# Performance work log

Measured on AMD Instinct MI355X. Metric: run time of the kernel, lower is better.

## Reference

```python
import jax, jax.numpy as jnp
import numpy as np

NUM_EXPERTS = 8
CAPACITY = 320  # per-batch per-expert token capacity


def setup_inputs() -> dict:
    key = jax.random.key(0)
    k0, k1, k2, k3 = jax.random.split(key, 4)
    B, S, D, F = 4, 2048, 1024, 4096
    E = NUM_EXPERTS
    hidden_states = jax.random.normal(k0, (B, S, D), dtype=jnp.float32)
    gate_w = jax.random.normal(k1, (E, D), dtype=jnp.float32) * 0.02
    w1 = jax.random.normal(k2, (E, D, F), dtype=jnp.float32) * 0.02
    w2 = jax.random.normal(k3, (E, F, D), dtype=jnp.float32) * 0.02
    return {"hidden_states": hidden_states, "gate_w": gate_w, "w1": w1, "w2": w2}


def reference(hidden_states, gate_w, w1, w2):
    E, C = NUM_EXPERTS, CAPACITY
    B, S, D = hidden_states.shape

    # --- route ---
    router_logits = jnp.einsum('bsd,ed->bse', hidden_states, gate_w)
    router_probs = jax.nn.softmax(router_logits, axis=-1)
    expert_idx = jnp.argmax(router_probs, axis=-1)                      # [B,S]
    onehot = jax.nn.one_hot(expert_idx, E, dtype=jnp.int32)             # [B,S,E]
    priority = jnp.cumsum(onehot, axis=1)                               # [B,S,E]
    router_mask = onehot * (priority <= C)                              # [B,S,E]
    assigned = jnp.sum(router_mask, axis=-1) > 0                        # [B,S]
    # slot within expert buffer; dropped tokens go to overflow slot C
    slot = jnp.where(assigned, jnp.sum(priority * onehot, axis=-1) - 1, C)  # [B,S]
    top_prob = jnp.max(router_probs, axis=-1, keepdims=True)            # [B,S,1]

    # --- dispatch: scatter tokens into [B,E,C+1,D] buffers ---
    def dispatch(x_b, e_b, s_b):
        return jnp.zeros((E, C + 1, D), x_b.dtype).at[e_b, s_b].set(x_b)
    buf = jax.vmap(dispatch)(hidden_states, expert_idx, slot)           # [B,E,C+1,D]

    # --- per-expert FFN as grouped GEMM ---
    h = jax.nn.silu(jnp.einsum('becd,edf->becf', buf, w1))
    y = jnp.einsum('becf,efd->becd', h, w2)                             # [B,E,C+1,D]

    # --- combine: gather expert outputs back to token order ---
    gathered = jax.vmap(lambda y_b, e_b, s_b: y_b[e_b, s_b])(y, expert_idx, slot)  # [B,S,D]
    next_states = jnp.where(assigned[..., None], gathered, hidden_states)
    out = top_prob * next_states

    # argmax of capacity-masked one-hot: dropped tokens -> expert 0
    expert_index = jnp.where(assigned, expert_idx, 0)
    return out, router_logits, expert_index
```

## Files before the change

kernel.cpp:

```cpp
#include <hip/hip_runtime.h>

#define B_  4
#define S_  2048
#define D_  1024
#define F_  4096
#define E_  8
#define C_  320
#define MPAD_ 1280
#define NT_ (B_*S_)
#define SLOT_ 49152

typedef short bf16x8 __attribute__((ext_vector_type(8)));
typedef float f32x4  __attribute__((ext_vector_type(4)));

using gptr_t = const __attribute__((address_space(1))) void*;
using lptr_t = __attribute__((address_space(3))) void*;

__device__ static inline void gll16(const void* g, void* l) {
    __builtin_amdgcn_global_load_lds((gptr_t)g, (lptr_t)l, 16, 0, 0);
}

__device__ static inline unsigned short f2b(float f) {
    unsigned int u = __float_as_uint(f);
    u += 0x7fffu + ((u >> 16) & 1u);
    return (unsigned short)(u >> 16);
}

__global__ __launch_bounds__(256) void k_convT(const float* __restrict__ in,
                                               unsigned short* __restrict__ out,
                                               int R, int Cc) {
    __shared__ unsigned short ld[64][66];
    int e = blockIdx.z;
    const float* src = in + (size_t)e * R * Cc;
    unsigned short* dst = out + (size_t)e * R * Cc;
    int c0 = blockIdx.x * 64, r0 = blockIdx.y * 64;
    int t = threadIdx.x;

    int rr = t >> 4;
    int cg = t & 15;
#pragma unroll
    for (int p = 0; p < 4; p++) {
        int row = p * 16 + rr;
        float4 v = *(const float4*)(src + (size_t)(r0 + row) * Cc + c0 + cg * 4);
        ld[cg * 4 + 0][row] = f2b(v.x);
        ld[cg * 4 + 1][row] = f2b(v.y);
        ld[cg * 4 + 2][row] = f2b(v.z);
        ld[cg * 4 + 3][row] = f2b(v.w);
    }
    __syncthreads();

    int cc = t >> 3;
    int rg = t & 7;
#pragma unroll
    for (int p = 0; p < 2; p++) {
        int col = p * 32 + cc;
        const unsigned* lp = (const unsigned*)&ld[col][rg * 8];
        uint4 w;
        w.x = lp[0]; w.y = lp[1]; w.z = lp[2]; w.w = lp[3];
        *(uint4*)(dst + (size_t)(c0 + col) * R + r0 + rg * 8) = w;
    }
}

__global__ __launch_bounds__(256) void k_router(const float* __restrict__ hs,
                                                const float* __restrict__ gw,
                                                float* __restrict__ logits,
                                                int* __restrict__ eidx,
                                                float* __restrict__ tp) {
    int tok  = (int)((blockIdx.x * 256 + threadIdx.x) >> 6);
    int lane = threadIdx.x & 63;
    const float* x = hs + (size_t)tok * D_;
    double acc[E_];
#pragma unroll
    for (int e = 0; e < E_; e++) acc[e] = 0.0;
    for (int i = 0; i < 16; i++) {
        float xv = x[lane + 64 * i];
#pragma unroll
        for (int e = 0; e < E_; e++)
            acc[e] += (double)xv * (double)gw[e * D_ + lane + 64 * i];
    }
#pragma unroll
    for (int e = 0; e < E_; e++) {
#pragma unroll
        for (int off = 32; off > 0; off >>= 1)
            acc[e] += __shfl_xor(acc[e], off, 64);
    }
    if (lane == 0) {
        float l[E_];
        float mx = -1e30f; int am = 0;
#pragma unroll
        for (int e = 0; e < E_; e++) {
            l[e] = (float)acc[e];
            if (l[e] > mx) { mx = l[e]; am = e; }
        }
        float se = 0.f;
#pragma unroll
        for (int e = 0; e < E_; e++) se += __expf(l[e] - mx);
        tp[tok]   = 1.0f / se;
        eidx[tok] = am;
#pragma unroll
        for (int e = 0; e < E_; e++) logits[(size_t)tok * E_ + e] = l[e];
    }
}

__global__ __launch_bounds__(256) void k_scan(const int* __restrict__ eidx,
                                              int* __restrict__ slot,
                                              int* __restrict__ tok_list,
                                              int* __restrict__ counts,
                                              float* __restrict__ eif) {
    int b = blockIdx.x;
    __shared__ int cCnt[32][E_];
    __shared__ int cBase[32][E_];
    int t = threadIdx.x, wv = t >> 6, lane = t & 63;
    const int* eb = eidx + b * S_;
    for (int c = wv; c < 32; c += 4) {
        int e = eb[c * 64 + lane];
#pragma unroll
        for (int x = 0; x < E_; x++) {
            unsigned long long m = __ballot(e == x);
            if (lane == 0) cCnt[c][x] = __popcll(m);
        }
    }
    __syncthreads();
    if (t < E_) {
        int s = 0;
        for (int c = 0; c < 32; c++) { cBase[c][t] = s; s += cCnt[c][t]; }
        counts[b * E_ + t] = s;
    }
    __syncthreads();
    for (int c = wv; c < 32; c += 4) {
        int s_tok = c * 64 + lane;
        int e = eb[s_tok];
        unsigned long long lowmask = (1ull << lane) - 1ull;
        int rank = 0;
#pragma unroll
        for (int x = 0; x < E_; x++) {
            unsigned long long m = __ballot(e == x);
            if (x == e) rank = __popcll(m & lowmask);
        }
        int pos = cBase[c][e] + rank;
        int assigned = (pos < C_);
        slot[b * S_ + s_tok] = assigned ? pos : C_;
        if (assigned) tok_list[(b * E_ + e) * C_ + pos] = s_tok;
        eif[b * S_ + s_tok] = assigned ? (float)e : 0.0f;
    }
}

__global__ void k_base(const int* __restrict__ counts,
                       int* __restrict__ ebase,
                       int* __restrict__ nE) {
    int e = threadIdx.x;
    if (e < E_) {
        int s = 0;
#pragma unroll
        for (int b = 0; b < B_; b++) {
            ebase[b * E_ + e] = s;
            s += min(counts[b * E_ + e], C_);
        }
        nE[e] = s;
    }
}

__global__ __launch_bounds__(256) void k_dispatch(const float* __restrict__ hs,
                                                  const int* __restrict__ tlB,
                                                  const int* __restrict__ ebase,
                                                  const int* __restrict__ nE,
                                                  int* __restrict__ tlG,
                                                  unsigned short* __restrict__ Xd) {
    int w    = (int)((blockIdx.x * 256 + threadIdx.x) >> 6);
    int lane = threadIdx.x & 63;
    int e = w / MPAD_, r = w - e * MPAD_;
    unsigned short* drow = Xd + ((size_t)e * MPAD_ + r) * D_;
    if (r < nE[e]) {
        int b = 0;
#pragma unroll
        for (int bb = 1; bb < B_; bb++) if (r >= ebase[bb * E_ + e]) b = bb;
        int pos = r - ebase[b * E_ + e];
        int ts  = tlB[(b * E_ + e) * C_ + pos];
        if (lane == 0) tlG[e * MPAD_ + r] = b * S_ + ts;
        const float* src = hs + ((size_t)b * S_ + ts) * D_;
#pragma unroll
        for (int i = 0; i < 2; i++) {
            int c0 = (lane + 64 * i) * 8;
            float4 v0 = *(const float4*)(src + c0);
            float4 v1 = *(const float4*)(src + c0 + 4);
            uint4 pk;
            pk.x = (unsigned)f2b(v0.x) | ((unsigned)f2b(v0.y) << 16);
            pk.y = (unsigned)f2b(v0.z) | ((unsigned)f2b(v0.w) << 16);
            pk.z = (unsigned)f2b(v1.x) | ((unsigned)f2b(v1.y) << 16);
            pk.w = (unsigned)f2b(v1.z) | ((unsigned)f2b(v1.w) << 16);
            *(uint4*)(drow + c0) = pk;
        }
    } else {
        uint4 zz = {0u, 0u, 0u, 0u};
#pragma unroll
        for (int i = 0; i < 2; i++)
            *(uint4*)(drow + (lane + 64 * i) * 8) = zz;
    }
}

template<int LDK, int KT>
__device__ __forceinline__ void gemm_core(const unsigned short* __restrict__ Ab,
                                          const unsigned short* __restrict__ Bb,
                                          char* sm, f32x4 (&acc)[4][4]) {
    const int t    = threadIdx.x;
    const int lane = t & 63;
    const int wv   = t >> 6;
    const int wm   = wv >> 1;
    const int wn   = wv & 1;

    const int sr  = t >> 3;
    const int scs = (t & 7) ^ (sr & 7);
    const unsigned short* aS = Ab + (size_t)sr * LDK + scs * 8;
    const unsigned short* bS = Bb + (size_t)sr * LDK + scs * 8;
    const int wvoff = wv * 1024;

    const int rl  = lane & 15;
    const int sw  = lane & 7;
    const int kg  = lane >> 4;
    const int sx0 = ((kg    ) ^ sw) << 4;
    const int sx1 = ((kg + 4) ^ sw) << 4;
    const int aro = (wm * 64 + rl) * 128;
    const int bro = (wn * 64 + rl) * 128;

#pragma unroll
    for (int g = 0; g < 2; g++) {
        char* L = sm + g * SLOT_;
        const unsigned short* aP = aS + (size_t)g * 64;
        const unsigned short* bP = bS + (size_t)g * 64;
#pragma unroll
        for (int j = 0; j < 4; j++) gll16(aP + (size_t)j * 64 * LDK, L + j * 8192 + wvoff);
#pragma unroll
        for (int j = 0; j < 2; j++) gll16(bP + (size_t)j * 64 * LDK, L + 32768 + j * 8192 + wvoff);
    }
    asm volatile("s_waitcnt vmcnt(6)" ::: "memory");
    __builtin_amdgcn_s_barrier();

    int cslot = 0;
#pragma unroll 1
    for (int kt = 0; kt < KT; ++kt) {
        const char* cs = sm + cslot * SLOT_;
        int ps = cslot + 2; if (ps >= 3) ps -= 3;
        char* L = sm + ps * SLOT_;

        if (kt + 2 < KT) {
            const unsigned short* aP = aS + (size_t)(kt + 2) * 64;
            const unsigned short* bP = bS + (size_t)(kt + 2) * 64;
#pragma unroll
            for (int j = 0; j < 4; j++) gll16(aP + (size_t)j * 64 * LDK, L + j * 8192 + wvoff);
#pragma unroll
            for (int j = 0; j < 2; j++) gll16(bP + (size_t)j * 64 * LDK, L + 32768 + j * 8192 + wvoff);
        }

        bf16x8 a0[4], b0[4], a1[4], b1[4];
#pragma unroll
        for (int i = 0; i < 4; i++) a0[i] = *(const bf16x8*)(cs + aro + i * 2048 + sx0);
#pragma unroll
        for (int j = 0; j < 4; j++) b0[j] = *(const bf16x8*)(cs + 32768 + bro + j * 2048 + sx0);
#pragma unroll
        for (int i = 0; i < 4; i++) a1[i] = *(const bf16x8*)(cs + aro + i * 2048 + sx1);
#pragma unroll
        for (int j = 0; j < 4; j++) b1[j] = *(const bf16x8*)(cs + 32768 + bro + j * 2048 + sx1);

        __builtin_amdgcn_s_setprio(1);
#pragma unroll
        for (int i = 0; i < 4; i++)
#pragma unroll
            for (int j = 0; j < 4; j++)
                acc[i][j] = __builtin_amdgcn_mfma_f32_16x16x32_bf16(a0[i], b0[j], acc[i][j], 0, 0, 0);
#pragma unroll
        for (int i = 0; i < 4; i++)
#pragma unroll
            for (int j = 0; j < 4; j++)
                acc[i][j] = __builtin_amdgcn_mfma_f32_16x16x32_bf16(a1[i], b1[j], acc[i][j], 0, 0, 0);
        __builtin_amdgcn_s_setprio(0);

        if (kt + 2 < KT)      { asm volatile("s_waitcnt vmcnt(6)" ::: "memory"); }
        else if (kt + 1 < KT) { asm volatile("s_waitcnt vmcnt(0)" ::: "memory"); }
        __builtin_amdgcn_s_barrier();

        cslot++; if (cslot >= 3) cslot = 0;
    }
}

__global__ __launch_bounds__(512, 2) void k_ffn1(const unsigned short* __restrict__ Xd,
                                                 const unsigned short* __restrict__ w1t,
                                                 const int* __restrict__ nE,
                                                 unsigned short* __restrict__ h) {
    __shared__ __align__(16) char sm[3 * SLOT_];
    int id  = blockIdx.x;
    int e   = id & 7;
    int rem = id >> 3;
    int mt  = rem % 5;
    int nt  = rem / 5;
    int m0  = mt * 256;
    if (m0 >= nE[e]) return;
    int n0  = nt * 128;

    f32x4 acc[4][4];
    f32x4 z = {0.f, 0.f, 0.f, 0.f};
#pragma unroll
    for (int i = 0; i < 4; i++)
#pragma unroll
        for (int j = 0; j < 4; j++) acc[i][j] = z;

    const unsigned short* Ab = Xd  + ((size_t)e * MPAD_ + m0) * D_;
    const unsigned short* Bb = w1t + ((size_t)e * F_    + n0) * D_;
    gemm_core<D_, D_ / 64>(Ab, Bb, sm, acc);

    int lane = threadIdx.x & 63, wv = threadIdx.x >> 6, wm = wv >> 1, wn = wv & 1;
    unsigned short* hb = h + (size_t)e * MPAD_ * F_;
    int rb = m0 + wm * 64 + ((lane >> 4) << 2);
    int cb = n0 + wn * 64 + (lane & 15);
#pragma unroll
    for (int i = 0; i < 4; i++)
#pragma unroll
        for (int r = 0; r < 4; r++) {
            unsigned short* hr = hb + (size_t)(rb + i * 16 + r) * F_ + cb;
#pragma unroll
            for (int j = 0; j < 4; j++) {
                float v = acc[i][j][r];
                v = v / (1.0f + __expf(-v));
                hr[j * 16] = f2b(v);
            }
        }
}

__global__ __launch_bounds__(512, 2) void k_ffn2(const unsigned short* __restrict__ h,
                                                 const unsigned short* __restrict__ w2t,
                                                 const int* __restrict__ nE,
                                                 const int* __restrict__ tlG,
                                                 const float* __restrict__ tp,
                                                 float* __restrict__ out) {
    __shared__ __align__(16) char sm[3 * SLOT_];
    int id  = blockIdx.x;
    int e   = id & 7;
    int rem = id >> 3;
    int mt  = rem % 5;
    int nt  = rem / 5;
    int m0  = mt * 256;
    int n   = nE[e];
    if (m0 >= n) return;
    int n0  = nt * 128;

    f32x4 acc[4][4];
    f32x4 z = {0.f, 0.f, 0.f, 0.f};
#pragma unroll
    for (int i = 0; i < 4; i++)
#pragma unroll
        for (int j = 0; j < 4; j++) acc[i][j] = z;

    const unsigned short* Ab = h   + ((size_t)e * MPAD_ + m0) * F_;
    const unsigned short* Bb = w2t + ((size_t)e * D_    + n0) * F_;
    gemm_core<F_, F_ / 64>(Ab, Bb, sm, acc);

    int lane = threadIdx.x & 63, wv = threadIdx.x >> 6, wm = wv >> 1, wn = wv & 1;
    const int* tl = tlG + e * MPAD_;
    int rb = m0 + wm * 64 + ((lane >> 4) << 2);
    int cb = n0 + wn * 64 + (lane & 15);
#pragma unroll
    for (int i = 0; i < 4; i++)
#pragma unroll
        for (int r = 0; r < 4; r++) {
            int row = rb + i * 16 + r;
            if (row < n) {
                int gt = tl[row];
                float sc = tp[gt];
                float* orow = out + (size_t)gt * D_ + cb;
#pragma unroll
                for (int j = 0; j < 4; j++)
                    orow[j * 16] = sc * acc[i][j][r];
            }
        }
}

__global__ __launch_bounds__(256) void k_pass(const float* __restrict__ hs,
                                              const int* __restrict__ slot,
                                              const float* __restrict__ tp,
                                              float* __restrict__ out) {
    int tok  = (int)((blockIdx.x * 256 + threadIdx.x) >> 6);
    int lane = threadIdx.x & 63;
    if (slot[tok] < C_) return;
    float sc = tp[tok];
    const float* src = hs + (size_t)tok * D_;
    float* dst = out + (size_t)tok * D_;
#pragma unroll
    for (int i = 0; i < 4; i++) {
        float4 v = *(const float4*)(src + (lane + 64 * i) * 4);
        v.x *= sc; v.y *= sc; v.z *= sc; v.w *= sc;
        *(float4*)(dst + (lane + 64 * i) * 4) = v;
    }
}

extern "C" void kernel_launch(void* const* d_in, const int* in_sizes, int n_in,
                              void* d_out, int out_size, void* d_ws, size_t ws_size,
                              hipStream_t stream) {
    const float* hs = (const float*)d_in[0];
    const float* gw = (const float*)d_in[1];
    const float* w1 = (const float*)d_in[2];
    const float* w2 = (const float*)d_in[3];

    float* out    = (float*)d_out;
    float* logits = out + (size_t)NT_ * D_;
    float* eif    = logits + (size_t)NT_ * E_;

    char* ws = (char*)d_ws;
    int*            eidx   = (int*)(ws + 0);
    int*            slot   = (int*)(ws + 65536);
    float*          tp     = (float*)(ws + 131072);
    int*            tlB    = (int*)(ws + 196608);
    int*            tlG    = (int*)(ws + 237568);
    int*            counts = (int*)(ws + 278528);
    int*            ebase  = (int*)(ws + 278784);
    int*            nE     = (int*)(ws + 279040);
    unsigned short* Xd     = (unsigned short*)(ws + 327680);
    unsigned short* w1t    = (unsigned short*)(ws + 33554432ull);
    unsigned short* w2t    = (unsigned short*)(ws + 100663296ull);
    unsigned short* hbuf   = (unsigned short*)(ws + 167772160ull);

    dim3 blk(256);
    k_convT<<<dim3(F_ / 64, D_ / 64, E_), blk, 0, stream>>>(w1, w1t, D_, F_);
    k_convT<<<dim3(D_ / 64, F_ / 64, E_), blk, 0, stream>>>(w2, w2t, F_, D_);
    k_router<<<dim3(NT_ / 4), blk, 0, stream>>>(hs, gw, logits, eidx, tp);
    k_scan<<<dim3(B_), blk, 0, stream>>>(eidx, slot, tlB, counts, eif);
    k_base<<<dim3(1), dim3(64), 0, stream>>>(counts, ebase, nE);
    k_dispatch<<<dim3(E_ * MPAD_ / 4), blk, 0, stream>>>(hs, tlB, ebase, nE, tlG, Xd);
    k_ffn1<<<dim3(1280), dim3(512), 0, stream>>>(Xd, w1t, nE, hbuf);
    k_ffn2<<<dim3(320), dim3(512), 0, stream>>>(hbuf, w2t, nE, tlG, tp, out);
    k_pass<<<dim3(NT_ / 4), blk, 0, stream>>>(hs, slot, tp, out);
}
```

Measured before the change: 588.3 us.

## Replace triple-buffered 256x128 GEMM tiles with single-buffer 128x128 tiles

Measured after the change: 536.2 us. -8.9%, faster.

```diff
diff --git a/kernel.cpp b/kernel.cpp
--- a/kernel.cpp
+++ b/kernel.cpp
@@ -8,7 +8,6 @@
 #define C_  320
 #define MPAD_ 1280
 #define NT_ (B_*S_)
-#define SLOT_ 49152
 
 typedef short bf16x8 __attribute__((ext_vector_type(8)));
 typedef float f32x4  __attribute__((ext_vector_type(4)));
@@ -212,6 +211,8 @@
     const int scs = (t & 7) ^ (sr & 7);
     const unsigned short* aS = Ab + (size_t)sr * LDK + scs * 8;
     const unsigned short* bS = Bb + (size_t)sr * LDK + scs * 8;
+    char* ldsA = sm;
+    char* ldsB = sm + 16384;
     const int wvoff = wv * 1024;
 
     const int rl  = lane & 15;
@@ -222,77 +223,50 @@
     const int aro = (wm * 64 + rl) * 128;
     const int bro = (wn * 64 + rl) * 128;
 
-#pragma unroll
-    for (int g = 0; g < 2; g++) {
-        char* L = sm + g * SLOT_;
-        const unsigned short* aP = aS + (size_t)g * 64;
-        const unsigned short* bP = bS + (size_t)g * 64;
-#pragma unroll
-        for (int j = 0; j < 4; j++) gll16(aP + (size_t)j * 64 * LDK, L + j * 8192 + wvoff);
-#pragma unroll
-        for (int j = 0; j < 2; j++) gll16(bP + (size_t)j * 64 * LDK, L + 32768 + j * 8192 + wvoff);
-    }
-    asm volatile("s_waitcnt vmcnt(6)" ::: "memory");
-    __builtin_amdgcn_s_barrier();
-
-    int cslot = 0;
 #pragma unroll 1
     for (int kt = 0; kt < KT; ++kt) {
-        const char* cs = sm + cslot * SLOT_;
-        int ps = cslot + 2; if (ps >= 3) ps -= 3;
-        char* L = sm + ps * SLOT_;
-
-        if (kt + 2 < KT) {
-            const unsigned short* aP = aS + (size_t)(kt + 2) * 64;
-            const unsigned short* bP = bS + (size_t)(kt + 2) * 64;
-#pragma unroll
-            for (int j = 0; j < 4; j++) gll16(aP + (size_t)j * 64 * LDK, L + j * 8192 + wvoff);
-#pragma unroll
-            for (int j = 0; j < 2; j++) gll16(bP + (size_t)j * 64 * LDK, L + 32768 + j * 8192 + wvoff);
-        }
-
-        bf16x8 a0[4], b0[4], a1[4], b1[4];
-#pragma unroll
-        for (int i = 0; i < 4; i++) a0[i] = *(const bf16x8*)(cs + aro + i * 2048 + sx0);
-#pragma unroll
-        for (int j = 0; j < 4; j++) b0[j] = *(const bf16x8*)(cs + 32768 + bro + j * 2048 + sx0);
-#pragma unroll
-        for (int i = 0; i < 4; i++) a1[i] = *(const bf16x8*)(cs + aro + i * 2048 + sx1);
-#pragma unroll
-        for (int j = 0; j < 4; j++) b1[j] = *(const bf16x8*)(cs + 32768 + bro + j * 2048 + sx1);
-
-        __builtin_amdgcn_s_setprio(1);
+        __syncthreads();
+        const unsigned short* aP = aS + kt * 64;
+        const unsigned short* bP = bS + kt * 64;
+#pragma unroll
+        for (int j = 0; j < 4; j++) gll16(aP + (size_t)(j * 32) * LDK, ldsA + j * 4096 + wvoff);
+#pragma unroll
+        for (int j = 0; j < 4; j++) gll16(bP + (size_t)(j * 32) * LDK, ldsB + j * 4096 + wvoff);
+        __syncthreads();
+
+        bf16x8 a[4], b[4];
+#pragma unroll
+        for (int i = 0; i < 4; i++) a[i] = *(const bf16x8*)(ldsA + aro + i * 2048 + sx0);
+#pragma unroll
+        for (int j = 0; j < 4; j++) b[j] = *(const bf16x8*)(ldsB + bro + j * 2048 + sx0);
 #pragma unroll
         for (int i = 0; i < 4; i++)
 #pragma unroll
             for (int j = 0; j < 4; j++)
-                acc[i][j] = __builtin_amdgcn_mfma_f32_16x16x32_bf16(a0[i], b0[j], acc[i][j], 0, 0, 0);
+                acc[i][j] = __builtin_amdgcn_mfma_f32_16x16x32_bf16(a[i], b[j], acc[i][j], 0, 0, 0);
+#pragma unroll
+        for (int i = 0; i < 4; i++) a[i] = *(const bf16x8*)(ldsA + aro + i * 2048 + sx1);
+#pragma unroll
+        for (int j = 0; j < 4; j++) b[j] = *(const bf16x8*)(ldsB + bro + j * 2048 + sx1);
 #pragma unroll
         for (int i = 0; i < 4; i++)
 #pragma unroll
             for (int j = 0; j < 4; j++)
-                acc[i][j] = __builtin_amdgcn_mfma_f32_16x16x32_bf16(a1[i], b1[j], acc[i][j], 0, 0, 0);
-        __builtin_amdgcn_s_setprio(0);
-
-        if (kt + 2 < KT)      { asm volatile("s_waitcnt vmcnt(6)" ::: "memory"); }
-        else if (kt + 1 < KT) { asm volatile("s_waitcnt vmcnt(0)" ::: "memory"); }
-        __builtin_amdgcn_s_barrier();
-
-        cslot++; if (cslot >= 3) cslot = 0;
-    }
-}
-
-__global__ __launch_bounds__(512, 2) void k_ffn1(const unsigned short* __restrict__ Xd,
+                acc[i][j] = __builtin_amdgcn_mfma_f32_16x16x32_bf16(a[i], b[j], acc[i][j], 0, 0, 0);
+    }
+}
+
+__global__ __launch_bounds__(256, 4) void k_ffn1(const unsigned short* __restrict__ Xd,
                                                  const unsigned short* __restrict__ w1t,
                                                  const int* __restrict__ nE,
                                                  unsigned short* __restrict__ h) {
-    __shared__ __align__(16) char sm[3 * SLOT_];
+    __shared__ __align__(16) char sm[32768];
     int id  = blockIdx.x;
     int e   = id & 7;
     int rem = id >> 3;
-    int mt  = rem % 5;
-    int nt  = rem / 5;
-    int m0  = mt * 256;
+    int mt  = rem % 10;
+    int nt  = rem / 10;
+    int m0  = mt * 128;
     if (m0 >= nE[e]) return;
     int n0  = nt * 128;
 
@@ -325,19 +299,19 @@
         }
 }
 
-__global__ __launch_bounds__(512, 2) void k_ffn2(const unsigned short* __restrict__ h,
+__global__ __launch_bounds__(256, 4) void k_ffn2(const unsigned short* __restrict__ h,
                                                  const unsigned short* __restrict__ w2t,
                                                  const int* __restrict__ nE,
                                                  const int* __restrict__ tlG,
                                                  const float* __restrict__ tp,
                                                  float* __restrict__ out) {
-    __shared__ __align__(16) char sm[3 * SLOT_];
+    __shared__ __align__(16) char sm[32768];
     int id  = blockIdx.x;
     int e   = id & 7;
     int rem = id >> 3;
-    int mt  = rem % 5;
-    int nt  = rem / 5;
-    int m0  = mt * 256;
+    int mt  = rem % 10;
+    int nt  = rem / 10;
+    int m0  = mt * 128;
     int n   = nE[e];
     if (m0 >= n) return;
     int n0  = nt * 128;
@@ -424,7 +398,7 @@
     k_scan<<<dim3(B_), blk, 0, stream>>>(eidx, slot, tlB, counts, eif);
     k_base<<<dim3(1), dim3(64), 0, stream>>>(counts, ebase, nE);
     k_dispatch<<<dim3(E_ * MPAD_ / 4), blk, 0, stream>>>(hs, tlB, ebase, nE, tlG, Xd);
-    k_ffn1<<<dim3(1280), dim3(512), 0, stream>>>(Xd, w1t, nE, hbuf);
-    k_ffn2<<<dim3(320), dim3(512), 0, stream>>>(hbuf, w2t, nE, tlG, tp, out);
+    k_ffn1<<<dim3(2560), blk, 0, stream>>>(Xd, w1t, nE, hbuf);
+    k_ffn2<<<dim3(640), blk, 0, stream>>>(hbuf, w2t, nE, tlG, tp, out);
     k_pass<<<dim3(NT_ / 4), blk, 0, stream>>>(hs, slot, tp, out);
 }
```
